# Kernel optimization log

Measured on AMD Instinct MI355X. Metric: run time of the kernel, lower is better.

The kernel has to match this reference:

```python
import jax, jax.numpy as jnp
import numpy as np

NUM_HEADS = 8
D_HEAD = 96
D_TIME = 64
NUM_BLOCKS = D_HEAD // 3
HALF_T = D_TIME // 2


def setup_inputs() -> dict:
    key = jax.random.key(0)
    ks = jax.random.split(key, 8)
    B, T, H, W = 2, 8, 64, 64
    q = jax.random.normal(ks[0], (B, T, NUM_HEADS, H, W, D_HEAD), dtype=jnp.float32)
    k = jax.random.normal(ks[1], (B, T, NUM_HEADS, H, W, D_HEAD), dtype=jnp.float32)
    # lat/lon in radians
    spatial_pos = jax.random.uniform(ks[2], (B, H, W, 2), dtype=jnp.float32) * jnp.pi - jnp.pi / 2
    time_pos = jax.random.uniform(ks[3], (B, T), dtype=jnp.float32) * 100.0
    freq_spatial = 0.02 * jax.random.normal(ks[4], (NUM_HEADS, NUM_BLOCKS, 2), dtype=jnp.float32)
    freq_temporal = 0.02 * jax.random.normal(ks[5], (HALF_T,), dtype=jnp.float32)
    Wt = jax.random.normal(ks[6], (D_HEAD, D_TIME), dtype=jnp.float32) / np.sqrt(D_TIME)
    bt = jax.random.normal(ks[7], (D_HEAD,), dtype=jnp.float32) * 0.01
    return {"q": q, "k": k, "spatial_pos": spatial_pos, "time_pos": time_pos,
            "freq_spatial": freq_spatial, "freq_temporal": freq_temporal,
            "Wt": Wt, "bt": bt}


def _spherical_angles(spatial_pos, freq_spatial):
    # spatial_pos: [B,H,W,2] (lat, lon); freq_spatial: [heads, blocks, 2]
    lat = spatial_pos[..., 0]  # [B,H,W]
    lon = spatial_pos[..., 1]
    fa = freq_spatial[..., 0]  # lon freq [heads, blocks]
    fb = freq_spatial[..., 1]  # lat freq
    # angles: [B, heads, H, W, blocks]
    A = lon[:, None, :, :, None] * fa[None, :, None, None, :]
    Bp = lat[:, None, :, :, None] * fb[None, :, None, None, :]
    return A, Bp


def _rotate(x, cosA, sinA, cosB, sinB):
    # x: [B,T,heads,H,W,blocks,3]; trig: [B,1,heads,H,W,blocks]
    x0, x1, x2 = x[..., 0], x[..., 1], x[..., 2]
    # row-vector times rotation matrix: out_j = sum_i x_i R[i, j]
    o0 = x0 * cosA + x1 * sinA
    o1 = -x0 * cosB * sinA + x1 * cosB * cosA + x2 * sinB
    o2 = x0 * sinB * sinA - x1 * sinB * cosA + x2 * cosB
    return jnp.stack([o0, o1, o2], axis=-1)


def reference(q, k, spatial_pos, time_pos, freq_spatial, freq_temporal, Wt, bt):
    B, T, heads, H, W, d = q.shape
    nb = d // 3
    A, Bp = _spherical_angles(spatial_pos, freq_spatial)  # [B,heads,H,W,blocks]
    cosA, sinA = jnp.cos(A)[:, None], jnp.sin(A)[:, None]
    cosB, sinB = jnp.cos(Bp)[:, None], jnp.sin(Bp)[:, None]
    qb = q.reshape(B, T, heads, H, W, nb, 3)
    kb = k.reshape(B, T, heads, H, W, nb, 3)
    q_rot = _rotate(qb, cosA, sinA, cosB, sinB).reshape(B, T, heads, H, W, d)
    k_rot = _rotate(kb, cosA, sinA, cosB, sinB).reshape(B, T, heads, H, W, d)
    # temporal RoPE embedding: interleave cos/sin -> [B,T,d_time]
    phase = time_pos[..., None] * freq_temporal  # [B,T,half]
    emb = jnp.stack([jnp.cos(phase), jnp.sin(phase)], axis=-1).reshape(B, T, -1)
    temp = emb @ Wt.T + bt  # [B,T,d_head]
    temp = temp[:, :, None, None, None, :]
    return q_rot + temp, k_rot + temp
```

## Files before the change

### kernel.cpp

```cpp
#include <hip/hip_runtime.h>
#include <math.h>

#define NB      32
#define NHEADS  8
#define DH      96
#define DT      64
#define HALFT   32
#define BB      2
#define TT      8
#define HH      64
#define WW      64

typedef float f32x4 __attribute__((ext_vector_type(4)));
typedef float f32x2 __attribute__((ext_vector_type(2)));

__global__ void temp_kernel(const float* __restrict__ time_pos,
                            const float* __restrict__ freq_temporal,
                            const float* __restrict__ Wt,
                            const float* __restrict__ bt,
                            float* __restrict__ temp) {
    const int row = blockIdx.x;
    const int d   = threadIdx.x;
    const float p = time_pos[row];
    const float* __restrict__ wrow = Wt + d * DT;
    float sum = bt[d];
    #pragma unroll
    for (int j = 0; j < HALFT; ++j) {
        float s, c;
        sincosf(p * freq_temporal[j], &s, &c);
        sum = fmaf(c, wrow[2 * j], sum);
        sum = fmaf(s, wrow[2 * j + 1], sum);
    }
    temp[row * DH + d] = sum;
}

__global__ __launch_bounds__(256) void rope_kernel(
        const float* __restrict__ q,
        const float* __restrict__ k,
        const float* __restrict__ spatial_pos,
        const float* __restrict__ freq_spatial,
        const float* __restrict__ temp,
        float* __restrict__ qo,
        float* __restrict__ ko) {
    const unsigned g = blockIdx.x * 256u + threadIdx.x;

    const int b4   = g & 7;
    const int x    = (g >> 3)  & 63;
    const int y    = (g >> 9)  & 63;
    const int head = (g >> 15) & 7;
    const int t    = (g >> 18) & 7;
    const int b    = (int)(g >> 21);

    const int sp = ((b * HH + y) * WW + x) * 2;
    const f32x2 ll = *(const f32x2*)(spatial_pos + sp);
    const float lat = ll[0], lon = ll[1];

    const f32x4* __restrict__ fptr =
        (const f32x4*)(freq_spatial + (head * NB + b4 * 4) * 2);
    const f32x4 f01 = fptr[0];
    const f32x4 f23 = fptr[1];
    const float fa[4] = { f01[0], f01[2], f23[0], f23[2] };
    const float fb[4] = { f01[1], f01[3], f23[1], f23[3] };

    const float* __restrict__ trow = temp + (b * TT + t) * DH + b4 * 12;
    float tv[12];
    {
        const f32x4 t0 = ((const f32x4*)trow)[0];
        const f32x4 t1 = ((const f32x4*)trow)[1];
        const f32x4 t2 = ((const f32x4*)trow)[2];
        #pragma unroll
        for (int c = 0; c < 4; ++c) {
            tv[c] = t0[c]; tv[4 + c] = t1[c]; tv[8 + c] = t2[c];
        }
    }

    const size_t e = (size_t)g * 12u;
    float qf[12], kf[12];
    {
        const f32x4* __restrict__ qp = (const f32x4*)(q + e);
        const f32x4* __restrict__ kp = (const f32x4*)(k + e);
        #pragma unroll
        for (int v = 0; v < 3; ++v) {
            const f32x4 qv = qp[v];
            const f32x4 kv = kp[v];
            #pragma unroll
            for (int c = 0; c < 4; ++c) {
                qf[4 * v + c] = qv[c];
                kf[4 * v + c] = kv[c];
            }
        }
    }

    float qr[12], kr[12];
    #pragma unroll
    for (int r = 0; r < 4; ++r) {
        float sA, cA, sB, cB;
        __sincosf(lon * fa[r], &sA, &cA);
        __sincosf(lat * fb[r], &sB, &cB);

        const float q0 = qf[3 * r], q1 = qf[3 * r + 1], q2 = qf[3 * r + 2];
        const float k0 = kf[3 * r], k1 = kf[3 * r + 1], k2 = kf[3 * r + 2];

        const float uq = q1 * cA - q0 * sA;
        qr[3 * r]     = q0 * cA + q1 * sA + tv[3 * r];
        qr[3 * r + 1] = cB * uq + q2 * sB + tv[3 * r + 1];
        qr[3 * r + 2] = -sB * uq + q2 * cB + tv[3 * r + 2];

        const float uk = k1 * cA - k0 * sA;
        kr[3 * r]     = k0 * cA + k1 * sA + tv[3 * r];
        kr[3 * r + 1] = cB * uk + k2 * sB + tv[3 * r + 1];
        kr[3 * r + 2] = -sB * uk + k2 * cB + tv[3 * r + 2];
    }

    {
        f32x4* __restrict__ qop = (f32x4*)(qo + e);
        f32x4* __restrict__ kop = (f32x4*)(ko + e);
        #pragma unroll
        for (int v = 0; v < 3; ++v) {
            f32x4 qv, kv;
            #pragma unroll
            for (int c = 0; c < 4; ++c) {
                qv[c] = qr[4 * v + c];
                kv[c] = kr[4 * v + c];
            }
            qop[v] = qv;
            kop[v] = kv;
        }
    }
}

extern "C" void kernel_launch(void* const* d_in, const int* in_sizes, int n_in,
                              void* d_out, int out_size, void* d_ws, size_t ws_size,
                              hipStream_t stream) {
    const float* q             = (const float*)d_in[0];
    const float* k             = (const float*)d_in[1];
    const float* spatial_pos   = (const float*)d_in[2];
    const float* time_pos      = (const float*)d_in[3];
    const float* freq_spatial  = (const float*)d_in[4];
    const float* freq_temporal = (const float*)d_in[5];
    const float* Wt            = (const float*)d_in[6];
    const float* bt            = (const float*)d_in[7];

    float* out  = (float*)d_out;
    float* temp = (float*)d_ws;

    temp_kernel<<<BB * TT, DH, 0, stream>>>(time_pos, freq_temporal, Wt, bt, temp);

    const unsigned n_groups = BB * TT * NHEADS * HH * WW * (NB / 4);
    const size_t per_tensor = (size_t)n_groups * 12u;
    rope_kernel<<<n_groups / 256, 256, 0, stream>>>(
        q, k, spatial_pos, freq_spatial, temp, out, out + per_tensor);
}
```

Measured before the change: 661.8 us.

## Stage q/k through LDS for fully coalesced loads and nontemporal stores

Each thread used to load and store 48 contiguous bytes as three strided float4 accesses. The kernel now has each block read a contiguous 3072-float tile in coalesced float4s, stage it in shared memory, and let each thread take its 12 floats from there. Results go back through LDS and are written coalesced with nontemporal stores, and q and k are processed one after the other to reuse the same buffer. The cost is extra LDS traffic and barriers, and the k load is issued only after q's barrier, which may reduce memory overlap.

```diff
diff --git a/kernel.cpp b/kernel.cpp
--- a/kernel.cpp
+++ b/kernel.cpp
@@ -42,7 +42,9 @@
         const float* __restrict__ temp,
         float* __restrict__ qo,
         float* __restrict__ ko) {
-    const unsigned g = blockIdx.x * 256u + threadIdx.x;
+    __shared__ f32x4 lds4[768];
+    const int tid = threadIdx.x;
+    const unsigned g = blockIdx.x * 256u + tid;
 
     const int b4   = g & 7;
     const int x    = (g >> 3)  & 63;
@@ -51,20 +53,31 @@
     const int t    = (g >> 18) & 7;
     const int b    = (int)(g >> 21);
 
+    const size_t base = (size_t)blockIdx.x * 3072u;
+
     const int sp = ((b * HH + y) * WW + x) * 2;
     const f32x2 ll = *(const f32x2*)(spatial_pos + sp);
     const float lat = ll[0], lon = ll[1];
 
     const f32x4* __restrict__ fptr =
-        (const f32x4*)(freq_spatial + (head * NB + b4 * 4) * 2);
+        (const f32x4*)(freq_spatial + head * 64 + b4 * 8);
     const f32x4 f01 = fptr[0];
     const f32x4 f23 = fptr[1];
-    const float fa[4] = { f01[0], f01[2], f23[0], f23[2] };
-    const float fb[4] = { f01[1], f01[3], f23[1], f23[3] };
 
-    const float* __restrict__ trow = temp + (b * TT + t) * DH + b4 * 12;
+    float sA[4], cA[4], sB[4], cB[4];
+    {
+        const float fa[4] = { f01[0], f01[2], f23[0], f23[2] };
+        const float fb[4] = { f01[1], f01[3], f23[1], f23[3] };
+        #pragma unroll
+        for (int r = 0; r < 4; ++r) {
+            __sincosf(lon * fa[r], &sA[r], &cA[r]);
+            __sincosf(lat * fb[r], &sB[r], &cB[r]);
+        }
+    }
+
     float tv[12];
     {
+        const float* __restrict__ trow = temp + (b * TT + t) * DH + b4 * 12;
         const f32x4 t0 = ((const f32x4*)trow)[0];
         const f32x4 t1 = ((const f32x4*)trow)[1];
         const f32x4 t2 = ((const f32x4*)trow)[2];
@@ -74,58 +87,56 @@
         }
     }
 
-    const size_t e = (size_t)g * 12u;
-    float qf[12], kf[12];
-    {
-        const f32x4* __restrict__ qp = (const f32x4*)(q + e);
-        const f32x4* __restrict__ kp = (const f32x4*)(k + e);
+    const float* __restrict__ srcs[2] = { q, k };
+    float*       __restrict__ dsts[2] = { qo, ko };
+
+    #pragma unroll
+    for (int s = 0; s < 2; ++s) {
+        const f32x4* __restrict__ gp = (const f32x4*)(srcs[s] + base);
+        const f32x4 st0 = gp[tid];
+        const f32x4 st1 = gp[tid + 256];
+        const f32x4 st2 = gp[tid + 512];
+
+        if (s) __syncthreads();
+
+        lds4[tid]       = st0;
+        lds4[tid + 256] = st1;
+        lds4[tid + 512] = st2;
+        __syncthreads();
+
+        const f32x4 a0 = lds4[tid * 3];
+        const f32x4 a1 = lds4[tid * 3 + 1];
+        const f32x4 a2 = lds4[tid * 3 + 2];
+        float xf[12];
         #pragma unroll
-        for (int v = 0; v < 3; ++v) {
-            const f32x4 qv = qp[v];
-            const f32x4 kv = kp[v];
-            #pragma unroll
-            for (int c = 0; c < 4; ++c) {
-                qf[4 * v + c] = qv[c];
-                kf[4 * v + c] = kv[c];
-            }
+        for (int c = 0; c < 4; ++c) {
+            xf[c] = a0[c]; xf[4 + c] = a1[c]; xf[8 + c] = a2[c];
         }
-    }
 
-    float qr[12], kr[12];
-    #pragma unroll
-    for (int r = 0; r < 4; ++r) {
-        float sA, cA, sB, cB;
-        __sincosf(lon * fa[r], &sA, &cA);
-        __sincosf(lat * fb[r], &sB, &cB);
+        float xr[12];
+        #pragma unroll
+        for (int r = 0; r < 4; ++r) {
+            const float x0 = xf[3 * r], x1 = xf[3 * r + 1], x2 = xf[3 * r + 2];
+            const float u = x1 * cA[r] - x0 * sA[r];
+            xr[3 * r]     = x0 * cA[r] + x1 * sA[r] + tv[3 * r];
+            xr[3 * r + 1] = cB[r] * u + x2 * sB[r] + tv[3 * r + 1];
+            xr[3 * r + 2] = -sB[r] * u + x2 * cB[r] + tv[3 * r + 2];
+        }
 
-        const float q0 = qf[3 * r], q1 = qf[3 * r + 1], q2 = qf[3 * r + 2];
-        const float k0 = kf[3 * r], k1 = kf[3 * r + 1], k2 = kf[3 * r + 2];
+        f32x4 r0, r1, r2;
+        #pragma unroll
+        for (int c = 0; c < 4; ++c) {
+            r0[c] = xr[c]; r1[c] = xr[4 + c]; r2[c] = xr[8 + c];
+        }
+        lds4[tid * 3]     = r0;
+        lds4[tid * 3 + 1] = r1;
+        lds4[tid * 3 + 2] = r2;
+        __syncthreads();
 
-        const float uq = q1 * cA - q0 * sA;
-        qr[3 * r]     = q0 * cA + q1 * sA + tv[3 * r];
-        qr[3 * r + 1] = cB * uq + q2 * sB + tv[3 * r + 1];
-        qr[3 * r + 2] = -sB * uq + q2 * cB + tv[3 * r + 2];
-
-        const float uk = k1 * cA - k0 * sA;
-        kr[3 * r]     = k0 * cA + k1 * sA + tv[3 * r];
-        kr[3 * r + 1] = cB * uk + k2 * sB + tv[3 * r + 1];
-        kr[3 * r + 2] = -sB * uk + k2 * cB + tv[3 * r + 2];
-    }
-
-    {
-        f32x4* __restrict__ qop = (f32x4*)(qo + e);
-        f32x4* __restrict__ kop = (f32x4*)(ko + e);
-        #pragma unroll
-        for (int v = 0; v < 3; ++v) {
-            f32x4 qv, kv;
-            #pragma unroll
-            for (int c = 0; c < 4; ++c) {
-                qv[c] = qr[4 * v + c];
-                kv[c] = kr[4 * v + c];
-            }
-            qop[v] = qv;
-            kop[v] = kv;
-        }
+        f32x4* __restrict__ op = (f32x4*)(dsts[s] + base);
+        __builtin_nontemporal_store(lds4[tid],       op + tid);
+        __builtin_nontemporal_store(lds4[tid + 256], op + tid + 256);
+        __builtin_nontemporal_store(lds4[tid + 512], op + tid + 512);
     }
 }
 
```

Result: no change. 666.6 us (+0.7%).
